# Kernel tuning notes

Measured on AMD Instinct MI355X. Metric: run time of the kernel, lower is better.

The kernel has to match this reference:

```python
import jax, jax.numpy as jnp
import numpy as np

B, C, H, W = 8, 4, 64, 2048
KH, KW = 3, 5
PH, PW = KH // 2, KW // 2
NUM_ITERS = 3
THETA_GAMMA = 0.9
THETA_ALPHA = 0.9
THETA_BETA = 0.015


def smoothness_kernel(theta):
    # Gaussian over squared window offsets, center zeroed, placed on class diagonal
    hs = jnp.arange(KH, dtype=jnp.float32) - KH // 2
    ws = jnp.arange(KW, dtype=jnp.float32) - KW // 2
    pdist = hs[:, None] ** 2 + ws[None, :] ** 2  # (KH,KW)
    k = jnp.exp(-pdist / (2.0 * theta ** 2))
    k = k.at[KH // 2, KW // 2].set(0.0)
    kernel = jnp.zeros((C, C, KH, KW), jnp.float32)
    kernel = kernel.at[jnp.arange(C), jnp.arange(C)].set(k)
    return kernel


def unfold_neighbors(x):
    # x: (b, c, H, W) -> (b, c, KH*KW-1, H*W), center tap excluded; row-major (kh,kw)
    b, c = x.shape[0], x.shape[1]
    xp = jnp.pad(x, ((0, 0), (0, 0), (PH, PH), (PW, PW)))
    taps = [xp[:, :, dh:dh + H, dw:dw + W]
            for dh in range(KH) for dw in range(KW)]
    K = KH * KW
    del taps[K // 2]  # exclude center pixel
    patches = jnp.stack(taps, axis=2)  # (b, c, K-1, H, W)
    return patches.reshape(b, c, K - 1, H * W)


def conv_same(x, kernel):
    return jax.lax.conv_general_dilated(
        x, kernel, window_strides=(1, 1), padding=[(PH, PH), (PW, PW)],
        dimension_numbers=('NCHW', 'OIHW', 'NCHW'))


def setup_inputs() -> dict:
    key = jax.random.key(0)
    k1, k2, k3 = jax.random.split(key, 3)
    unary = jax.random.normal(k1, (B, C, H, W), jnp.float32)
    xyz = jax.random.normal(k2, (B, 3, H, W), jnp.float32)
    mask = (jax.random.uniform(k3, (B, H, W)) > 0.1).astype(jnp.float32)
    weight_appearance = jnp.ones((1, C, 1, 1), jnp.float32) * 0.1
    weight_smoothness = jnp.ones((1, C, 1, 1), jnp.float32) * 0.02
    compat_w = 1.0 - jnp.eye(C, dtype=jnp.float32)  # Potts label compatibility (O,I)
    return {
        'unary': unary, 'xyz': xyz, 'mask': mask,
        'weight_appearance': weight_appearance,
        'weight_smoothness': weight_smoothness,
        'compat_w': compat_w,
    }


def reference(unary, xyz, mask, weight_appearance, weight_smoothness, compat_w):
    kernel_gamma = smoothness_kernel(THETA_GAMMA)
    kernel_alpha = smoothness_kernel(THETA_ALPHA)
    theta_beta = jnp.full((C,), THETA_BETA, jnp.float32)

    # precompute appearance (bilateral) kernel from xyz; detached in the original
    anchor = xyz.reshape(B, 3, 1, H * W)
    nb = unfold_neighbors(xyz)  # (B,3,14,HW)
    pdist = ((nb - anchor) ** 2).sum(axis=1, keepdims=True)  # (B,1,14,HW)
    kernel_beta = jnp.exp(-pdist / (2.0 * theta_beta[None, :, None, None] ** 2))  # (B,C,14,HW)
    kernel_beta = jax.lax.stop_gradient(kernel_beta)

    m = mask[:, None]  # (B,1,H,W)
    Q = unary
    for _ in range(NUM_ITERS):
        Q = jax.nn.softmax(Q, axis=1)
        k_smooth = conv_same(Q, kernel_gamma)
        # appearance message passing: masked windowed gather weighted by kernel_beta
        masked_Q = Q * m
        Q_nb = unfold_neighbors(masked_Q)  # (B,C,14,HW)
        exp_app = (Q_nb * kernel_beta).sum(axis=2).reshape(B, C, H, W) * m
        exp_smooth = conv_same(Q, kernel_alpha)
        k_app = exp_app * exp_smooth
        weighted_k = weight_smoothness * k_smooth + weight_appearance * k_app
        pairwise = jnp.einsum('oc,bchw->bohw', compat_w, weighted_k)
        Q = unary - pairwise
    return Q
```

## Files before the change

### kernel.cpp

```cpp
#include <hip/hip_runtime.h>

#define Bsz 8
#define Cn  4
#define Hn  64
#define Wn  2048
#define HW  (Hn*Wn)

#define TW 64
#define TH 8
#define BW 76
#define BH 14
#define NB (BW*BH)

#define G1 0.53940824f
#define G2 0.29096127f
#define G4 0.08465836f
#define G5 0.04566536f

__device__ __forceinline__ float4 f4fma(float a, const float4& v, const float4& acc) {
    return make_float4(fmaf(a, v.x, acc.x), fmaf(a, v.y, acc.y),
                       fmaf(a, v.z, acc.z), fmaf(a, v.w, acc.w));
}

template<bool FINAL>
__device__ __forceinline__ void finish_px(int gh, int gw, int bidx,
                                          const float4& ksm, const float4& app, float mc,
                                          const float* __restrict__ unary,
                                          float* __restrict__ outp,
                                          float4* __restrict__ Sout, size_t qbase,
                                          const float* wa, const float* wsm,
                                          const float* cw) {
    bool inimg = (gh >= 0) & (gh < Hn) & (gw >= 0) & (gw < Wn);
    if (inimg) {
        size_t p = (size_t)gh * Wn + gw;
        float wk0 = ksm.x * (wsm[0] + wa[0] * (app.x * mc));
        float wk1 = ksm.y * (wsm[1] + wa[1] * (app.y * mc));
        float wk2 = ksm.z * (wsm[2] + wa[2] * (app.z * mc));
        float wk3 = ksm.w * (wsm[3] + wa[3] * (app.w * mc));
        float q[4];
#pragma unroll
        for (int o = 0; o < 4; ++o) {
            float pw = cw[o * 4 + 0] * wk0 + cw[o * 4 + 1] * wk1 +
                       cw[o * 4 + 2] * wk2 + cw[o * 4 + 3] * wk3;
            q[o] = unary[qbase + p + (size_t)o * HW] - pw;
        }
        if (FINAL) {
#pragma unroll
            for (int o = 0; o < 4; ++o)
                outp[qbase + p + (size_t)o * HW] = q[o];
        } else {
            float mx = fmaxf(fmaxf(q[0], q[1]), fmaxf(q[2], q[3]));
            float e0 = __expf(q[0] - mx), e1 = __expf(q[1] - mx);
            float e2 = __expf(q[2] - mx), e3 = __expf(q[3] - mx);
            float inv = 1.0f / (e0 + e1 + e2 + e3);
            Sout[bidx] = make_float4(e0 * inv, e1 * inv, e2 * inv, e3 * inv);
        }
    } else if (!FINAL) {
        Sout[bidx] = make_float4(0.f, 0.f, 0.f, 0.f);
    }
}

template<int RW, int RH, int OY, int OX, bool FINAL>
__device__ __forceinline__ void do_iter(const float4* __restrict__ Sin,
                                        float4* __restrict__ Sout,
                                        const float4* __restrict__ X,
                                        const float* __restrict__ unary,
                                        float* __restrict__ outp,
                                        size_t qbase, int h0, int w0, int tid,
                                        const float* wa, const float* wsm,
                                        const float* cw) {
    const float Gt[3][5] = {
        {G5, G2, G1, G2, G5},
        {G4, G1, 0.f, G1, G4},
        {G5, G2, G1, G2, G5}};
    constexpr int P = RW * (RH / 2);
    for (int i = tid; i < P; i += 256) {
        int pr = i / RW;
        int pc = i - pr * RW;
        int r0 = OY + 2 * pr;
        int c  = OX + pc;
        int b0 = (r0 + 3) * BW + (c + 6);

        float4 xc0 = X[b0];
        float4 xc1 = X[b0 + BW];
        float4 ksm0 = make_float4(0,0,0,0), app0 = make_float4(0,0,0,0);
        float4 ksm1 = make_float4(0,0,0,0), app1 = make_float4(0,0,0,0);

#pragma unroll
        for (int j = 0; j < 4; ++j) {
            int rb = b0 + (j - 1) * BW;
            float4 s[5], x[5];
#pragma unroll
            for (int d = 0; d < 5; ++d) {
                s[d] = Sin[rb + d - 2];
                x[d] = X[rb + d - 2];
            }
#pragma unroll
            for (int d = 0; d < 5; ++d) {
                if (j <= 2 && !(j == 1 && d == 2)) {
                    ksm0 = f4fma(Gt[j][d], s[d], ksm0);
                    float dx = x[d].x - xc0.x, dy = x[d].y - xc0.y, dz = x[d].z - xc0.z;
                    float bm = __expf(-2222.2222f * (dx*dx + dy*dy + dz*dz)) * x[d].w;
                    app0 = f4fma(bm, s[d], app0);
                }
                if (j >= 1 && !(j == 2 && d == 2)) {
                    ksm1 = f4fma(Gt[j - 1][d], s[d], ksm1);
                    float dx = x[d].x - xc1.x, dy = x[d].y - xc1.y, dz = x[d].z - xc1.z;
                    float bm = __expf(-2222.2222f * (dx*dx + dy*dy + dz*dz)) * x[d].w;
                    app1 = f4fma(bm, s[d], app1);
                }
            }
        }

        int gw = w0 + c;
        int gh0 = h0 + r0;
        finish_px<FINAL>(gh0,     gw, b0,      ksm0, app0, xc0.w, unary, outp, Sout,
                         qbase, wa, wsm, cw);
        finish_px<FINAL>(gh0 + 1, gw, b0 + BW, ksm1, app1, xc1.w, unary, outp, Sout,
                         qbase, wa, wsm, cw);
    }
}

__global__ __launch_bounds__(256, 3) void crf_fused(const float* __restrict__ unary,
                                                    const float* __restrict__ xyz,
                                                    const float* __restrict__ mask,
                                                    const float* __restrict__ wa_g,
                                                    const float* __restrict__ wsm_g,
                                                    const float* __restrict__ cw_g,
                                                    float* __restrict__ outp) {
    __shared__ float4 SA[NB];
    __shared__ float4 SB[NB];
    __shared__ float4 X[NB];

    const int tid = threadIdx.x;
    const int w0 = blockIdx.x * TW;
    const int h0 = blockIdx.y * TH;
    const int b  = blockIdx.z;

    const size_t qbase = (size_t)b * Cn * HW;
    const size_t xbase = (size_t)b * 3 * HW;
    const size_t mbase = (size_t)b * HW;

    float wa[4], wsm[4], cw[16];
#pragma unroll
    for (int k = 0; k < 4; ++k) { wa[k] = wa_g[k]; wsm[k] = wsm_g[k]; }
#pragma unroll
    for (int k = 0; k < 16; ++k) cw[k] = cw_g[k];

    for (int i = tid; i < NB; i += 256) {
        int br = i / BW;
        int bc = i - br * BW;
        int gh = h0 + br - 3;
        int gw = w0 + bc - 6;
        float4 s  = make_float4(0.f, 0.f, 0.f, 0.f);
        float4 xm = make_float4(0.f, 0.f, 0.f, 0.f);
        if (gh >= 0 && gh < Hn && gw >= 0 && gw < Wn) {
            size_t p = (size_t)gh * Wn + gw;
            float q0 = unary[qbase + p];
            float q1 = unary[qbase + p + HW];
            float q2 = unary[qbase + p + 2 * HW];
            float q3 = unary[qbase + p + 3 * HW];
            float mx = fmaxf(fmaxf(q0, q1), fmaxf(q2, q3));
            float e0 = __expf(q0 - mx), e1 = __expf(q1 - mx);
            float e2 = __expf(q2 - mx), e3 = __expf(q3 - mx);
            float inv = 1.0f / (e0 + e1 + e2 + e3);
            s = make_float4(e0 * inv, e1 * inv, e2 * inv, e3 * inv);
            xm = make_float4(xyz[xbase + p], xyz[xbase + p + HW],
                             xyz[xbase + p + 2 * HW], mask[mbase + p]);
        }
        SA[i] = s;
        X[i] = xm;
    }
    __syncthreads();

    do_iter<72, 12, -2, -4, false>(SA, SB, X, unary, nullptr, qbase, h0, w0, tid, wa, wsm, cw);
    __syncthreads();
    do_iter<68, 10, -1, -2, false>(SB, SA, X, unary, nullptr, qbase, h0, w0, tid, wa, wsm, cw);
    __syncthreads();
    do_iter<64,  8,  0,  0, true >(SA, nullptr, X, unary, outp, qbase, h0, w0, tid, wa, wsm, cw);
}

extern "C" void kernel_launch(void* const* d_in, const int* in_sizes, int n_in,
                              void* d_out, int out_size, void* d_ws, size_t ws_size,
                              hipStream_t stream) {
    const float* unary  = (const float*)d_in[0];
    const float* xyz    = (const float*)d_in[1];
    const float* mask   = (const float*)d_in[2];
    const float* wa     = (const float*)d_in[3];
    const float* wsm    = (const float*)d_in[4];
    const float* compat = (const float*)d_in[5];
    float* outp = (float*)d_out;

    dim3 grid(Wn / TW, Hn / TH, Bsz), blk(256);
    crf_fused<<<grid, blk, 0, stream>>>(unary, xyz, mask, wa, wsm, compat, outp);
}
```

Measured before the change: 138.9 us.

## Precompute bilateral weights once in LDS and use fp16 packed math

```diff
diff --git a/kernel.cpp b/kernel.cpp
--- a/kernel.cpp
+++ b/kernel.cpp
@@ -1,4 +1,5 @@
 #include <hip/hip_runtime.h>
+#include <hip/hip_fp16.h>
 
 #define Bsz 8
 #define Cn  4
@@ -11,37 +12,53 @@
 #define BW 76
 #define BH 14
 #define NB (BW*BH)
+#define R1W 72
+#define R1H 12
+#define NR1 (R1W*R1H)
+
+#define XBYTES (NB*16)
+#define BBYTES (4*NR1*8)
 
 #define G1 0.53940824f
 #define G2 0.29096127f
 #define G4 0.08465836f
 #define G5 0.04566536f
 
-__device__ __forceinline__ float4 f4fma(float a, const float4& v, const float4& acc) {
-    return make_float4(fmaf(a, v.x, acc.x), fmaf(a, v.y, acc.y),
-                       fmaf(a, v.z, acc.z), fmaf(a, v.w, acc.w));
+struct Half4 { __half2 lo, hi; };
+
+__device__ __forceinline__ __half hsel(const Half4& h, int k) {
+    return (k == 0) ? __low2half(h.lo) : (k == 1) ? __high2half(h.lo)
+         : (k == 2) ? __low2half(h.hi) : __high2half(h.hi);
+}
+
+__device__ __forceinline__ __half2 GH2(int r, int d) {
+    const float Gt[3][5] = {
+        {G5, G2, G1, G2, G5},
+        {G4, G1, 0.f, G1, G4},
+        {G5, G2, G1, G2, G5}};
+    return __float2half2_rn(Gt[r][d]);
 }
 
 template<bool FINAL>
-__device__ __forceinline__ void finish_px(int gh, int gw, int bidx,
-                                          const float4& ksm, const float4& app, float mc,
-                                          const float* __restrict__ unary,
-                                          float* __restrict__ outp,
-                                          float4* __restrict__ Sout, size_t qbase,
-                                          const float* wa, const float* wsm,
-                                          const float* cw) {
+__device__ __forceinline__ void finish_px(int gh, int gw, int bi,
+        __half2 ka, __half2 kb, __half2 aa, __half2 ab, __half mch,
+        const float* __restrict__ unary, float* __restrict__ outp,
+        Half4* __restrict__ Sout, size_t qbase,
+        const float* wa, const float* wsm, const float* cw) {
     bool inimg = (gh >= 0) & (gh < Hn) & (gw >= 0) & (gw < Wn);
     if (inimg) {
         size_t p = (size_t)gh * Wn + gw;
-        float wk0 = ksm.x * (wsm[0] + wa[0] * (app.x * mc));
-        float wk1 = ksm.y * (wsm[1] + wa[1] * (app.y * mc));
-        float wk2 = ksm.z * (wsm[2] + wa[2] * (app.z * mc));
-        float wk3 = ksm.w * (wsm[3] + wa[3] * (app.w * mc));
+        float ksm[4] = {__low2float(ka), __high2float(ka), __low2float(kb), __high2float(kb)};
+        float app[4] = {__low2float(aa), __high2float(aa), __low2float(ab), __high2float(ab)};
+        float mc = __half2float(mch);
+        float wk[4];
+#pragma unroll
+        for (int c = 0; c < 4; ++c)
+            wk[c] = ksm[c] * (wsm[c] + wa[c] * (app[c] * mc));
         float q[4];
 #pragma unroll
         for (int o = 0; o < 4; ++o) {
-            float pw = cw[o * 4 + 0] * wk0 + cw[o * 4 + 1] * wk1 +
-                       cw[o * 4 + 2] * wk2 + cw[o * 4 + 3] * wk3;
+            float pw = cw[o*4+0]*wk[0] + cw[o*4+1]*wk[1] + cw[o*4+2]*wk[2] + cw[o*4+3]*wk[3];
             q[o] = unary[qbase + p + (size_t)o * HW] - pw;
         }
         if (FINAL) {
@@ -50,74 +67,83 @@
                 outp[qbase + p + (size_t)o * HW] = q[o];
         } else {
             float mx = fmaxf(fmaxf(q[0], q[1]), fmaxf(q[2], q[3]));
-            float e0 = __expf(q[0] - mx), e1 = __expf(q[1] - mx);
-            float e2 = __expf(q[2] - mx), e3 = __expf(q[3] - mx);
+            float e0 = __expf(q[0]-mx), e1 = __expf(q[1]-mx);
+            float e2 = __expf(q[2]-mx), e3 = __expf(q[3]-mx);
             float inv = 1.0f / (e0 + e1 + e2 + e3);
-            Sout[bidx] = make_float4(e0 * inv, e1 * inv, e2 * inv, e3 * inv);
+            Half4 s; s.lo = __floats2half2_rn(e0*inv, e1*inv);
+            s.hi = __floats2half2_rn(e2*inv, e3*inv);
+            Sout[bi] = s;
         }
     } else if (!FINAL) {
-        Sout[bidx] = make_float4(0.f, 0.f, 0.f, 0.f);
+        Half4 z; z.lo = __float2half2_rn(0.f); z.hi = z.lo;
+        Sout[bi] = z;
     }
 }
 
 template<int RW, int RH, int OY, int OX, bool FINAL>
-__device__ __forceinline__ void do_iter(const float4* __restrict__ Sin,
-                                        float4* __restrict__ Sout,
-                                        const float4* __restrict__ X,
+__device__ __forceinline__ void do_iter(const Half4* __restrict__ Sin,
+                                        Half4* __restrict__ Sout,
+                                        const Half4* __restrict__ BETA,
                                         const float* __restrict__ unary,
                                         float* __restrict__ outp,
                                         size_t qbase, int h0, int w0, int tid,
                                         const float* wa, const float* wsm,
                                         const float* cw) {
-    const float Gt[3][5] = {
-        {G5, G2, G1, G2, G5},
-        {G4, G1, 0.f, G1, G4},
-        {G5, G2, G1, G2, G5}};
     constexpr int P = RW * (RH / 2);
     for (int i = tid; i < P; i += 256) {
         int pr = i / RW;
         int pc = i - pr * RW;
-        int r0 = OY + 2 * pr;
-        int c  = OX + pc;
-        int b0 = (r0 + 3) * BW + (c + 6);
-
-        float4 xc0 = X[b0];
-        float4 xc1 = X[b0 + BW];
-        float4 ksm0 = make_float4(0,0,0,0), app0 = make_float4(0,0,0,0);
-        float4 ksm1 = make_float4(0,0,0,0), app1 = make_float4(0,0,0,0);
+        const int r0 = OY + 2 * pr;
+        const int c  = OX + pc;
+        const int bi0 = (r0 + 3) * BW + (c + 6);
+        const int p1  = (r0 + 2) * R1W + (c + 4);
+
+        Half4 B0[4], B1[4];
+#pragma unroll
+        for (int g = 0; g < 4; ++g) {
+            B0[g] = BETA[g * NR1 + p1];
+            B1[g] = BETA[g * NR1 + p1 + R1W];
+        }
+
+        const __half2 z2 = __float2half2_rn(0.f);
+        __half2 k0a = z2, k0b = z2, a0a = z2, a0b = z2;
+        __half2 k1a = z2, k1b = z2, a1a = z2, a1b = z2;
 
 #pragma unroll
         for (int j = 0; j < 4; ++j) {
-            int rb = b0 + (j - 1) * BW;
-            float4 s[5], x[5];
-#pragma unroll
-            for (int d = 0; d < 5; ++d) {
-                s[d] = Sin[rb + d - 2];
-                x[d] = X[rb + d - 2];
-            }
+            const int rb = bi0 + (j - 1) * BW;
+            Half4 s[5];
+#pragma unroll
+            for (int d = 0; d < 5; ++d) s[d] = Sin[rb + d - 2];
 #pragma unroll
             for (int d = 0; d < 5; ++d) {
                 if (j <= 2 && !(j == 1 && d == 2)) {
-                    ksm0 = f4fma(Gt[j][d], s[d], ksm0);
-                    float dx = x[d].x - xc0.x, dy = x[d].y - xc0.y, dz = x[d].z - xc0.z;
-                    float bm = __expf(-2222.2222f * (dx*dx + dy*dy + dz*dz)) * x[d].w;
-                    app0 = f4fma(bm, s[d], app0);
+                    const int t = (j == 0) ? d : (j == 1) ? ((d < 2) ? 5 + d : 4 + d) : 9 + d;
+                    const __half2 g2 = GH2(j, d);
+                    k0a = __hfma2(g2, s[d].lo, k0a);
+                    k0b = __hfma2(g2, s[d].hi, k0b);
+                    const __half2 bm2 = __half2half2(hsel(B0[t >> 2], t & 3));
+                    a0a = __hfma2(bm2, s[d].lo, a0a);
+                    a0b = __hfma2(bm2, s[d].hi, a0b);
                 }
                 if (j >= 1 && !(j == 2 && d == 2)) {
-                    ksm1 = f4fma(Gt[j - 1][d], s[d], ksm1);
-                    float dx = x[d].x - xc1.x, dy = x[d].y - xc1.y, dz = x[d].z - xc1.z;
-                    float bm = __expf(-2222.2222f * (dx*dx + dy*dy + dz*dz)) * x[d].w;
-                    app1 = f4fma(bm, s[d], app1);
+                    const int t = (j == 1) ? d : (j == 2) ? ((d < 2) ? 5 + d : 4 + d) : 9 + d;
+                    const __half2 g2 = GH2(j - 1, d);
+                    k1a = __hfma2(g2, s[d].lo, k1a);
+                    k1b = __hfma2(g2, s[d].hi, k1b);
+                    const __half2 bm2 = __half2half2(hsel(B1[t >> 2], t & 3));
+                    a1a = __hfma2(bm2, s[d].lo, a1a);
+                    a1b = __hfma2(bm2, s[d].hi, a1b);
                 }
             }
         }
 
-        int gw = w0 + c;
-        int gh0 = h0 + r0;
-        finish_px<FINAL>(gh0,     gw, b0,      ksm0, app0, xc0.w, unary, outp, Sout,
-                         qbase, wa, wsm, cw);
-        finish_px<FINAL>(gh0 + 1, gw, b0 + BW, ksm1, app1, xc1.w, unary, outp, Sout,
-                         qbase, wa, wsm, cw);
+        const int gw = w0 + c;
+        const int gh0 = h0 + r0;
+        finish_px<FINAL>(gh0,     gw, bi0,      k0a, k0b, a0a, a0b, hsel(B0[3], 2),
+                         unary, outp, Sout, qbase, wa, wsm, cw);
+        finish_px<FINAL>(gh0 + 1, gw, bi0 + BW, k1a, k1b, a1a, a1b, hsel(B1[3], 2),
+                         unary, outp, Sout, qbase, wa, wsm, cw);
     }
 }
 
@@ -128,9 +154,11 @@
                                                     const float* __restrict__ wsm_g,
                                                     const float* __restrict__ cw_g,
                                                     float* __restrict__ outp) {
-    __shared__ float4 SA[NB];
-    __shared__ float4 SB[NB];
-    __shared__ float4 X[NB];
+    __shared__ __align__(16) unsigned char LDS_[XBYTES + BBYTES];
+    Half4*  SA   = (Half4*)LDS_;
+    Half4*  SB   = SA + NB;
+    float4* XBUF = (float4*)LDS_;
+    Half4*  BETA = (Half4*)(LDS_ + XBYTES);
 
     const int tid = threadIdx.x;
     const int w0 = blockIdx.x * TW;
@@ -148,12 +176,48 @@
     for (int k = 0; k < 16; ++k) cw[k] = cw_g[k];
 
     for (int i = tid; i < NB; i += 256) {
-        int br = i / BW;
-        int bc = i - br * BW;
-        int gh = h0 + br - 3;
-        int gw = w0 + bc - 6;
-        float4 s  = make_float4(0.f, 0.f, 0.f, 0.f);
+        int br = i / BW, bc = i - br * BW;
+        int gh = h0 + br - 3, gw = w0 + bc - 6;
         float4 xm = make_float4(0.f, 0.f, 0.f, 0.f);
+        if (gh >= 0 && gh < Hn && gw >= 0 && gw < Wn) {
+            size_t p = (size_t)gh * Wn + gw;
+            xm = make_float4(xyz[xbase + p], xyz[xbase + p + HW],
+                             xyz[xbase + p + 2 * HW], mask[mbase + p]);
+        }
+        XBUF[i] = xm;
+    }
+    __syncthreads();
+
+    for (int p = tid; p < NR1; p += 256) {
+        int r1 = p / R1W, c1 = p - r1 * R1W;
+        int bi = (r1 + 1) * BW + (c1 + 2);
+        float4 xc = XBUF[bi];
+        float bm[14];
+        int t = 0;
+#pragma unroll
+        for (int dh = -1; dh <= 1; ++dh) {
+#pragma unroll
+            for (int dw = -2; dw <= 2; ++dw) {
+                if (dh == 0 && dw == 0) continue;
+                float4 xn = XBUF[bi + dh * BW + dw];
+                float dx = xn.x - xc.x, dy = xn.y - xc.y, dz = xn.z - xc.z;
+                bm[t++] = __expf(-2222.2222f * (dx*dx + dy*dy + dz*dz)) * xn.w;
+            }
+        }
+        Half4 g0, g1, g2, g3;
+        g0.lo = __floats2half2_rn(bm[0],  bm[1]);  g0.hi = __floats2half2_rn(bm[2],  bm[3]);
+        g1.lo = __floats2half2_rn(bm[4],  bm[5]);  g1.hi = __floats2half2_rn(bm[6],  bm[7]);
+        g2.lo = __floats2half2_rn(bm[8],  bm[9]);  g2.hi = __floats2half2_rn(bm[10], bm[11]);
+        g3.lo = __floats2half2_rn(bm[12], bm[13]); g3.hi = __floats2half2_rn(xc.w, 0.f);
+        BETA[0 * NR1 + p] = g0; BETA[1 * NR1 + p] = g1;
+        BETA[2 * NR1 + p] = g2; BETA[3 * NR1 + p] = g3;
+    }
+    __syncthreads();
+
+    for (int i = tid; i < NB; i += 256) {
+        int br = i / BW, bc = i - br * BW;
+        int gh = h0 + br - 3, gw = w0 + bc - 6;
+        Half4 s; s.lo = __float2half2_rn(0.f); s.hi = s.lo;
         if (gh >= 0 && gh < Hn && gw >= 0 && gw < Wn) {
             size_t p = (size_t)gh * Wn + gw;
             float q0 = unary[qbase + p];
@@ -164,20 +228,18 @@
             float e0 = __expf(q0 - mx), e1 = __expf(q1 - mx);
             float e2 = __expf(q2 - mx), e3 = __expf(q3 - mx);
             float inv = 1.0f / (e0 + e1 + e2 + e3);
-            s = make_float4(e0 * inv, e1 * inv, e2 * inv, e3 * inv);
-            xm = make_float4(xyz[xbase + p], xyz[xbase + p + HW],
-                             xyz[xbase + p + 2 * HW], mask[mbase + p]);
+            s.lo = __floats2half2_rn(e0 * inv, e1 * inv);
+            s.hi = __floats2half2_rn(e2 * inv, e3 * inv);
         }
         SA[i] = s;
-        X[i] = xm;
-    }
-    __syncthreads();
-
-    do_iter<72, 12, -2, -4, false>(SA, SB, X, unary, nullptr, qbase, h0, w0, tid, wa, wsm, cw);
-    __syncthreads();
-    do_iter<68, 10, -1, -2, false>(SB, SA, X, unary, nullptr, qbase, h0, w0, tid, wa, wsm, cw);
-    __syncthreads();
-    do_iter<64,  8,  0,  0, true >(SA, nullptr, X, unary, outp, qbase, h0, w0, tid, wa, wsm, cw);
+    }
+    __syncthreads();
+
+    do_iter<R1W, R1H, -2, -4, false>(SA, SB, BETA, unary, nullptr, qbase, h0, w0, tid, wa, wsm, cw);
+    __syncthreads();
+    do_iter<68, 10, -1, -2, false>(SB, SA, BETA, unary, nullptr, qbase, h0, w0, tid, wa, wsm, cw);
+    __syncthreads();
+    do_iter<64, 8, 0, 0, true>(SA, nullptr, BETA, unary, outp, qbase, h0, w0, tid, wa, wsm, cw);
 }
 
 extern "C" void kernel_launch(void* const* d_in, const int* in_sizes, int n_in,
```

New measurement: 123.4 us. 1.13x faster.
